# Kernel optimization log

Hardware: AMD Instinct MI355X
Metric: run time of the kernel (lower is better)

The kernel has to match this reference:

```python
import jax, jax.numpy as jnp
import numpy as np

N = 50000          # nodes
E = 800000         # edges (before self-loops)
DIN = 1024         # input_dim_mel
HID = 128          # hidden_dim
HEADS = 2
NC = 4             # num_classes
NEG_SLOPE = 0.2    # PyG GATConv default


def setup_inputs() -> dict:
    key = jax.random.key(0)
    ks = jax.random.split(key, 12)
    s = 0.05
    return {
        "x": jax.random.normal(ks[0], (N, DIN), dtype=jnp.float32),
        "edge_index": jax.random.randint(ks[1], (2, E), 0, N, dtype=jnp.int64),
        # linear_pre (stored as [in, out])
        "W_pre": jax.random.normal(ks[2], (DIN, HID), dtype=jnp.float32) * s,
        "b_pre": jnp.zeros((HID,), dtype=jnp.float32),
        # gat1: GATConv(HID, HID, heads=2, concat=True)
        "W1": jax.random.normal(ks[3], (HID, HEADS * HID), dtype=jnp.float32) * s,
        "a_src1": jax.random.normal(ks[4], (HEADS, HID), dtype=jnp.float32) * s,
        "a_dst1": jax.random.normal(ks[5], (HEADS, HID), dtype=jnp.float32) * s,
        "b1": jnp.zeros((HEADS * HID,), dtype=jnp.float32),
        # gat2: GATConv(HID*HEADS, NC, heads=1, concat=True)
        "W2": jax.random.normal(ks[6], (HEADS * HID, NC), dtype=jnp.float32) * s,
        "a_src2": jax.random.normal(ks[7], (1, NC), dtype=jnp.float32) * s,
        "a_dst2": jax.random.normal(ks[8], (1, NC), dtype=jnp.float32) * s,
        "b2": jnp.zeros((NC,), dtype=jnp.float32),
    }


def _gat_conv(x, W, a_src, a_dst, bias, src, dst, heads, out_ch):
    """PyG GATConv (concat=True, self-loops already appended to src/dst)."""
    n = x.shape[0]
    h = (x @ W).reshape(n, heads, out_ch)            # [N,H,C]
    alpha_src = (h * a_src).sum(-1)                  # [N,H]
    alpha_dst = (h * a_dst).sum(-1)                  # [N,H]
    e = alpha_src[src] + alpha_dst[dst]              # [E,H] edge scores
    e = jax.nn.leaky_relu(e, NEG_SLOPE)
    # segment softmax over incoming edges of each dst node
    m = jax.ops.segment_max(e, dst, num_segments=n)  # [N,H]
    e = jnp.exp(e - m[dst])
    s = jax.ops.segment_sum(e, dst, num_segments=n)  # [N,H]
    alpha = e / (s[dst] + 1e-16)                     # [E,H]
    # gather src messages, weight by attention, scatter-add to dst
    out = jax.ops.segment_sum(h[src] * alpha[:, :, None], dst, num_segments=n)
    return out.reshape(n, heads * out_ch) + bias


def reference(x, edge_index, W_pre, b_pre, W1, a_src1, a_dst1, b1,
              W2, a_src2, a_dst2, b2):
    n = x.shape[0]
    # add self-loops (PyG GATConv default)
    loops = jnp.arange(n, dtype=edge_index.dtype)
    src = jnp.concatenate([edge_index[0], loops])
    dst = jnp.concatenate([edge_index[1], loops])

    h = jax.nn.relu(x @ W_pre + b_pre)                               # [N,HID]
    h = jax.nn.elu(_gat_conv(h, W1, a_src1, a_dst1, b1, src, dst, HEADS, HID))
    out = _gat_conv(h, W2, a_src2, a_dst2, b2, src, dst, 1, NC)      # [N,NC]
    return out
```

## Files before the change

kernel.cpp:

```cpp
#include <hip/hip_runtime.h>
#include <hip/hip_bf16.h>

#define NEG_SLOPE 0.2f

typedef _Float16 f16x8 __attribute__((ext_vector_type(8)));
typedef _Float16 f16x4 __attribute__((ext_vector_type(4)));
typedef float f32x4 __attribute__((ext_vector_type(4)));
typedef unsigned short ushort_t;

#define AS_GLOBAL(p) ((const __attribute__((address_space(1))) void*)(p))
#define AS_SHARED(p) ((__attribute__((address_space(3))) void*)(p))


__global__ void khist(const int* __restrict__ dst, int E, int* __restrict__ counts) {
    int i = blockIdx.x * blockDim.x + threadIdx.x;
    if (i < E) atomicAdd(&counts[dst[i]], 1);
}

__global__ __launch_bounds__(1024) void kscan_part(const int* __restrict__ counts,
                                                   int* __restrict__ row_ptr,
                                                   int* __restrict__ bsum, int n) {
    __shared__ int wsum[16];
    int t = threadIdx.x, lane = t & 63, wid = t >> 6;
    int i = blockIdx.x * 1024 + t;
    int v = (i < n) ? (counts[i] + 1) : 0;
    int x = v;
    #pragma unroll
    for (int off = 1; off < 64; off <<= 1) {
        int y = __shfl_up(x, off, 64);
        if (lane >= off) x += y;
    }
    if (lane == 63) wsum[wid] = x;
    __syncthreads();
    if (wid == 0) {
        int ws = (lane < 16) ? wsum[lane] : 0;
        #pragma unroll
        for (int off = 1; off < 16; off <<= 1) {
            int y = __shfl_up(ws, off, 64);
            if (lane >= off) ws += y;
        }
        if (lane < 16) wsum[lane] = ws;
    }
    __syncthreads();
    int wave_excl = (wid == 0) ? 0 : wsum[wid - 1];
    if (i < n) row_ptr[i] = wave_excl + (x - v);
    if (t == 0) bsum[blockIdx.x] = wsum[15];
}

__global__ void kscan_tops(const int* __restrict__ bsum, int* __restrict__ boff,
                           int* __restrict__ row_ptr, int G, int n) {
    int lane = threadIdx.x;
    int v = (lane < G) ? bsum[lane] : 0;
    int x = v;
    #pragma unroll
    for (int off = 1; off < 64; off <<= 1) {
        int y = __shfl_up(x, off, 64);
        if (lane >= off) x += y;
    }
    if (lane < G) boff[lane] = x - v;
    if (lane == 63) row_ptr[n] = x;
}

__global__ void kscan_add(int* __restrict__ row_ptr, const int* __restrict__ boff,
                          int* __restrict__ cursor, int n) {
    int i = blockIdx.x * blockDim.x + threadIdx.x;
    if (i < n) {
        int r = row_ptr[i] + boff[i >> 10];
        row_ptr[i] = r;
        cursor[i] = r;
    }
}

__global__ void kfill(const int* __restrict__ src, const int* __restrict__ dst,
                      int E, int n, int* __restrict__ cursor, int* __restrict__ edge_src) {
    int i = blockIdx.x * blockDim.x + threadIdx.x;
    if (i < E) {
        int p = atomicAdd(&cursor[dst[i]], 1);
        edge_src[p] = src[i];
    } else if (i < E + n) {
        int v = i - E;
        int p = atomicAdd(&cursor[v], 1);
        edge_src[p] = v;
    }
}

__global__ void kprep(const float* __restrict__ Wpre, const float* __restrict__ W1,
                      ushort_t* __restrict__ PreF, ushort_t* __restrict__ W1h) {
    int i = blockIdx.x * blockDim.x + threadIdx.x;
    if (i < 1024 * 128) {
        int k = i >> 7, n = i & 127;
        int d = ((k >> 3) * 128 + n) * 8 + (k & 7);
        PreF[d] = __builtin_bit_cast(ushort_t, (_Float16)Wpre[i]);
    } else if (i < 1024 * 128 + 128 * 256) {
        int j2 = i - 1024 * 128;
        int k = j2 >> 8, n = j2 & 255;
        int d = ((k >> 3) * 256 + n) * 8 + (k & 7);
        W1h[d] = __builtin_bit_cast(ushort_t, (_Float16)W1[j2]);
    }
}

__device__ inline f16x4 cvt4(float4 v) {
    f16x4 r;
    r[0] = (_Float16)v.x; r[1] = (_Float16)v.y;
    r[2] = (_Float16)v.z; r[3] = (_Float16)v.w;
    return r;
}

__global__ __launch_bounds__(256) void kgemm_mfma1(const float* __restrict__ A,
                                                   const ushort_t* __restrict__ Bf,
                                                   const float* __restrict__ bias,
                                                   ushort_t* __restrict__ C, int M) {
    __shared__ __align__(16) ushort_t Bs[8192];
    __shared__ __align__(16) ushort_t As[2048];
    int t = threadIdx.x;
    int wid = t >> 6, lane = t & 63, q = lane >> 4, l15 = lane & 15;
    int wr = wid & 1, wc = wid >> 1;
    int m0 = blockIdx.x * 32;

    int ar = t >> 3, ac = t & 7;
    int srow = m0 + ar;
    if (srow >= M) srow = M - 1;
    const float* sA = A + (size_t)srow * 1024;
    int sw = ar & 7;
    int wadr0 = ar * 64 + (((ac >> 1)) ^ sw) * 8 + (ac & 1) * 4;
    int wadr1 = ar * 64 + ((4 + (ac >> 1)) ^ sw) * 8 + (ac & 1) * 4;

    float4 av[2][2];
    av[0][0] = *(const float4*)(sA + ac * 4);
    av[0][1] = *(const float4*)(sA + 32 + ac * 4);

    f32x4 acc[4];
    #pragma unroll
    for (int c = 0; c < 4; ++c) acc[c] = (f32x4){0.f, 0.f, 0.f, 0.f};

    int arow_rd = (wr * 16 + l15) * 64;
    int asw = l15 & 7;

    #pragma unroll 2
    for (int kt = 0; kt < 16; ++kt) {
        int cur = kt & 1, nxt = cur ^ 1;
        __syncthreads();
        {
            const ushort_t* sF = Bf + kt * 8192;
            #pragma unroll
            for (int i = 0; i < 4; ++i) {
                int ge = (i * 256 + t) * 8;
                int le = (i * 256 + (t & 0xC0)) * 8;
                __builtin_amdgcn_global_load_lds(AS_GLOBAL(sF + ge), AS_SHARED(Bs + le), 16, 0, 0);
            }
        }
        if (kt < 15) {
            const float* a2 = sA + (kt + 1) * 64;
            av[nxt][0] = *(const float4*)(a2 + ac * 4);
            av[nxt][1] = *(const float4*)(a2 + 32 + ac * 4);
        }
        *(f16x4*)(As + wadr0) = cvt4(av[cur][0]);
        *(f16x4*)(As + wadr1) = cvt4(av[cur][1]);
        __syncthreads();
        #pragma unroll
        for (int ks = 0; ks < 2; ++ks) {
            int kc = ks * 4 + q;
            f16x8 af = *(const f16x8*)(As + arow_rd + ((kc ^ asw) * 8));
            #pragma unroll
            for (int c = 0; c < 4; ++c) {
                f16x8 b = *(const f16x8*)(Bs + (kc * 128 + wc * 64 + c * 16 + l15) * 8);
                acc[c] = __builtin_amdgcn_mfma_f32_16x16x32_f16(af, b, acc[c], 0, 0, 0);
            }
        }
    }
    #pragma unroll
    for (int c = 0; c < 4; ++c) {
        int n = wc * 64 + c * 16 + l15;
        float bv = bias[n];
        #pragma unroll
        for (int r = 0; r < 4; ++r) {
            int mm = m0 + wr * 16 + q * 4 + r;
            if (mm < M)
                C[(size_t)mm * 128 + n] =
                    __builtin_bit_cast(ushort_t, (_Float16)fmaxf(acc[c][r] + bv, 0.f));
        }
    }
}

__global__ __launch_bounds__(256) void kgemm_mfma2(const ushort_t* __restrict__ Ah,
                                                   const ushort_t* __restrict__ W1h,
                                                   const float* __restrict__ a_src,
                                                   const float* __restrict__ a_dst,
                                                   ushort_t* __restrict__ C,
                                                   float* __restrict__ as1,
                                                   float* __restrict__ ad1, int M) {
    __shared__ __align__(16) ushort_t Bs[16384];
    int t = threadIdx.x;
    int wid = t >> 6, lane = t & 63;
    int q = lane >> 4, l15 = lane & 15;
    int g = blockIdx.y;
    int m0 = blockIdx.x * 64 + wid * 16;
    int m = m0 + l15;
    const ushort_t* arow = Ah + (size_t)(m < M ? m : 0) * 128;

    {
        #pragma unroll
        for (int i = 0; i < 8; ++i) {
            int j = i * 4 + wid;
            int kc = j >> 1, hk = j & 1;
            int ge = ((kc * 256) + g * 128 + hk * 64 + lane) * 8;
            int le = j * 512;
            __builtin_amdgcn_global_load_lds(AS_GLOBAL(W1h + ge), AS_SHARED(Bs + le), 16, 0, 0);
        }
    }
    f16x8 af[4];
    #pragma unroll
    for (int ks = 0; ks < 4; ++ks)
        af[ks] = *(const f16x8*)(arow + ks * 32 + q * 8);
    __syncthreads();

    f32x4 acc[8];
    #pragma unroll
    for (int c = 0; c < 8; ++c) acc[c] = (f32x4){0.f, 0.f, 0.f, 0.f};

    #pragma unroll
    for (int ks = 0; ks < 4; ++ks) {
        int kc = ks * 4 + q;
        #pragma unroll
        for (int c = 0; c < 8; ++c) {
            f16x8 b = *(const f16x8*)(Bs + (kc * 128 + c * 16 + l15) * 8);
            acc[c] = __builtin_amdgcn_mfma_f32_16x16x32_f16(af[ks], b, acc[c], 0, 0, 0);
        }
    }
    #pragma unroll
    for (int c = 0; c < 8; ++c) {
        int n = g * 128 + c * 16 + l15;
        #pragma unroll
        for (int r = 0; r < 4; ++r) {
            int mm = m0 + q * 4 + r;
            if (mm < M)
                C[(size_t)mm * 256 + n] = __builtin_bit_cast(ushort_t, (_Float16)acc[c][r]);
        }
    }
    float asv[4] = {0.f, 0.f, 0.f, 0.f};
    float adv[4] = {0.f, 0.f, 0.f, 0.f};
    #pragma unroll
    for (int c = 0; c < 8; ++c) {
        float sa = a_src[g * 128 + c * 16 + l15];
        float da = a_dst[g * 128 + c * 16 + l15];
        #pragma unroll
        for (int r = 0; r < 4; ++r) {
            asv[r] += acc[c][r] * sa;
            adv[r] += acc[c][r] * da;
        }
    }
    #pragma unroll
    for (int off = 1; off <= 8; off <<= 1) {
        #pragma unroll
        for (int r = 0; r < 4; ++r) {
            asv[r] += __shfl_xor(asv[r], off, 64);
            adv[r] += __shfl_xor(adv[r], off, 64);
        }
    }
    if (l15 == 0) {
        #pragma unroll
        for (int r = 0; r < 4; ++r) {
            int node = m0 + q * 4 + r;
            if (node < M) {
                as1[node * 2 + g] = asv[r];
                ad1[node * 2 + g] = adv[r];
            }
        }
    }
}

__global__ __launch_bounds__(128) void kagg1(const ushort_t* __restrict__ h1h,
                                             const float* __restrict__ as1,
                                             const float* __restrict__ ad1,
                                             const float* __restrict__ b1,
                                             const float* __restrict__ W2,
                                             const float* __restrict__ a_src2,
                                             const float* __restrict__ a_dst2,
                                             const int* __restrict__ row_ptr,
                                             const int* __restrict__ edge_src,
                                             float* __restrict__ h2,
                                             float* __restrict__ as2,
                                             float* __restrict__ ad2, int n) {
    __shared__ float w_lds[128];
    __shared__ int   s_lds[64];
    __shared__ float red[2][4];
    int node = blockIdx.x;
    int t = threadIdx.x;
    int wid = t >> 6;
    int beg = row_ptr[node], end = row_ptr[node + 1];
    int h_ch = t >> 6;
    float advv = ad1[node * 2 + (t & 1)];
    float acc0 = 0.f, acc1 = 0.f, ssum = 0.f;
    for (int base = beg; base < end; base += 64) {
        int cnt = min(64, end - base);
        int i = t >> 1, h = t & 1;
        if (i < cnt) {
            int s = edge_src[base + i];
            float e = as1[s * 2 + h] + advv;
            e = (e > 0.f) ? e : NEG_SLOPE * e;
            w_lds[i * 2 + h] = __expf(e);
            if (h == 0) s_lds[i] = s;
        }
        __syncthreads();
        #pragma unroll 4
        for (int i2 = 0; i2 < cnt; ++i2) {
            float wv = w_lds[i2 * 2 + h_ch];
            int s = s_lds[i2];
            unsigned p = *(const unsigned*)(h1h + (size_t)s * 256 + t * 2);
            _Float16 lo16 = __builtin_bit_cast(_Float16, (ushort_t)(p & 0xffffu));
            _Float16 hi16 = __builtin_bit_cast(_Float16, (ushort_t)(p >> 16));
            acc0 += wv * (float)lo16;
            acc1 += wv * (float)hi16;
            ssum += wv;
        }
        __syncthreads();
    }
    float inv = 1.f / (ssum + 1e-16f);
    float o0 = acc0 * inv + b1[t * 2];
    float o1 = acc1 * inv + b1[t * 2 + 1];
    o0 = (o0 > 0.f) ? o0 : (__expf(o0) - 1.f);
    o1 = (o1 > 0.f) ? o1 : (__expf(o1) - 1.f);
    float4 w0 = *(const float4*)(W2 + t * 8);
    float4 w1 = *(const float4*)(W2 + t * 8 + 4);
    float p0 = o0 * w0.x + o1 * w1.x;
    float p1 = o0 * w0.y + o1 * w1.y;
    float p2 = o0 * w0.z + o1 * w1.z;
    float p3 = o0 * w0.w + o1 * w1.w;
    #pragma unroll
    for (int off = 1; off < 64; off <<= 1) {
        p0 += __shfl_xor(p0, off, 64);
        p1 += __shfl_xor(p1, off, 64);
        p2 += __shfl_xor(p2, off, 64);
        p3 += __shfl_xor(p3, off, 64);
    }
    if ((t & 63) == 0) {
        red[wid][0] = p0; red[wid][1] = p1; red[wid][2] = p2; red[wid][3] = p3;
    }
    __syncthreads();
    if (t == 0) {
        float hv[4], s2 = 0.f, d2 = 0.f;
        #pragma unroll
        for (int j = 0; j < 4; ++j) {
            hv[j] = red[0][j] + red[1][j];
            h2[node * 4 + j] = hv[j];
            s2 += hv[j] * a_src2[j];
            d2 += hv[j] * a_dst2[j];
        }
        as2[node] = s2;
        ad2[node] = d2;
    }
}

__global__ __launch_bounds__(256) void kagg2(const float* __restrict__ h2,
                                             const float* __restrict__ as2,
                                             const float* __restrict__ ad2,
                                             const float* __restrict__ b2,
                                             const int* __restrict__ row_ptr,
                                             const int* __restrict__ edge_src,
                                             float* __restrict__ out, int n) {
    int wid = threadIdx.x >> 6, lane = threadIdx.x & 63;
    int node = blockIdx.x * 4 + wid;
    if (node >= n) return;
    int beg = row_ptr[node], end = row_ptr[node + 1];
    int j = lane & 3, ig = lane >> 2;
    float adv = ad2[node];
    float acc = 0.f, ssum = 0.f;
    for (int p = beg + ig; p < end; p += 16) {
        int s = edge_src[p];
        float e = as2[s] + adv;
        e = (e > 0.f) ? e : NEG_SLOPE * e;
        float wv = __expf(e);
        acc += wv * h2[s * 4 + j];
        ssum += wv;
    }
    #pragma unroll
    for (int off = 32; off >= 4; off >>= 1) {
        acc += __shfl_down(acc, off);
        ssum += __shfl_down(ssum, off);
    }
    if (lane < 4) out[node * 4 + j] = acc / (ssum + 1e-16f) + b2[j];
}

extern "C" void kernel_launch(void* const* d_in, const int* in_sizes, int n_in,
                              void* d_out, int out_size, void* d_ws, size_t ws_size,
                              hipStream_t stream) {
    const float* x      = (const float*)d_in[0];
    const int*   ei     = (const int*)d_in[1];
    const float* W_pre  = (const float*)d_in[2];
    const float* b_pre  = (const float*)d_in[3];
    const float* W1     = (const float*)d_in[4];
    const float* a_src1 = (const float*)d_in[5];
    const float* a_dst1 = (const float*)d_in[6];
    const float* b1     = (const float*)d_in[7];
    const float* W2     = (const float*)d_in[8];
    const float* a_src2 = (const float*)d_in[9];
    const float* a_dst2 = (const float*)d_in[10];
    const float* b2     = (const float*)d_in[11];
    float* out = (float*)d_out;

    const int DIN = 1024;
    const int E = in_sizes[1] / 2;
    const int N = in_sizes[0] / DIN;

    const int* esrc = ei;
    const int* edst = ei + E;

    char* ws = (char*)d_ws;
    size_t off = 0;
    ushort_t* h1h = (ushort_t*)(ws + off); off += (size_t)N * 256 * 2;
    ushort_t* h0h = (ushort_t*)(ws + off); off += (size_t)N * 128 * 2;
    float* as1 = (float*)(ws + off);  off += (size_t)N * 2 * 4;
    float* ad1 = (float*)(ws + off);  off += (size_t)N * 2 * 4;
    float* h2  = (float*)(ws + off);  off += (size_t)N * 4 * 4;
    float* as2 = (float*)(ws + off);  off += (size_t)N * 4;
    float* ad2 = (float*)(ws + off);  off += (size_t)N * 4;
    int* row_ptr = (int*)(ws + off);  off += ((size_t)N + 16) * 4;
    int* cursor  = (int*)(ws + off);  off += (size_t)N * 4;
    int* counts  = (int*)(ws + off);  off += (size_t)N * 4;
    int* bsum    = (int*)(ws + off);  off += 64 * 4;
    int* boff    = (int*)(ws + off);  off += 64 * 4;
    int* edge_src = (int*)(ws + off); off += (size_t)(E + N) * 4;
    ushort_t* PreF = (ushort_t*)(ws + off); off += 1024 * 128 * 2;
    ushort_t* W1h  = (ushort_t*)(ws + off); off += 128 * 256 * 2;

    int G = (N + 1023) / 1024;

    kprep<<<640, 256, 0, stream>>>(W_pre, W1, PreF, W1h);
    hipMemsetAsync(counts, 0, (size_t)N * 4, stream);
    khist<<<(E + 255) / 256, 256, 0, stream>>>(edst, E, counts);
    kscan_part<<<G, 1024, 0, stream>>>(counts, row_ptr, bsum, N);
    kscan_tops<<<1, 64, 0, stream>>>(bsum, boff, row_ptr, G, N);
    kscan_add<<<(N + 255) / 256, 256, 0, stream>>>(row_ptr, boff, cursor, N);
    kfill<<<(E + N + 255) / 256, 256, 0, stream>>>(esrc, edst, E, N, cursor, edge_src);

    int Mb32 = (N + 31) / 32;
    kgemm_mfma1<<<Mb32, 256, 0, stream>>>(x, PreF, b_pre, h0h, N);
    {
        int Mb = (N + 63) / 64;
        dim3 grid(Mb, 2);
        kgemm_mfma2<<<grid, 256, 0, stream>>>(h0h, W1h, a_src1, a_dst1, h1h, as1, ad1, N);
    }
    kagg1<<<N, 128, 0, stream>>>(h1h, as1, ad1, b1, W2, a_src2, a_dst2,
                                 row_ptr, edge_src, h2, as2, ad2, N);
    kagg2<<<(N + 3) / 4, 256, 0, stream>>>(h2, as2, ad2, b2, row_ptr, edge_src, out, N);
}
```

Before: 521.6 us.

## Process one node per wavefront in GAT layer-1 aggregation using shuffles

The first aggregation kernel now assigns one 64-lane wavefront per destination node instead of a 128-thread block. Each lane gathers four fp16 channels with an 8-byte load, and edge weights and source indices are broadcast with wave shuffles instead of LDS. This removes block-level barriers and the LDS reduction, and packs four nodes per 256-thread block to cut block scheduling overhead. Each lane now holds more accumulators, and the gather per edge stays a single 512-byte row read.

```diff
diff --git a/kernel.cpp b/kernel.cpp
--- a/kernel.cpp
+++ b/kernel.cpp
@@ -269,7 +269,7 @@
     }
 }
 
-__global__ __launch_bounds__(128) void kagg1(const ushort_t* __restrict__ h1h,
+__global__ __launch_bounds__(256) void kagg1(const ushort_t* __restrict__ h1h,
                                              const float* __restrict__ as1,
                                              const float* __restrict__ ad1,
                                              const float* __restrict__ b1,
@@ -281,51 +281,56 @@
                                              float* __restrict__ h2,
                                              float* __restrict__ as2,
                                              float* __restrict__ ad2, int n) {
-    __shared__ float w_lds[128];
-    __shared__ int   s_lds[64];
-    __shared__ float red[2][4];
-    int node = blockIdx.x;
-    int t = threadIdx.x;
-    int wid = t >> 6;
+    int wid = threadIdx.x >> 6, lane = threadIdx.x & 63;
+    int node = blockIdx.x * 4 + wid;
+    if (node >= n) return;
     int beg = row_ptr[node], end = row_ptr[node + 1];
-    int h_ch = t >> 6;
-    float advv = ad1[node * 2 + (t & 1)];
-    float acc0 = 0.f, acc1 = 0.f, ssum = 0.f;
-    for (int base = beg; base < end; base += 64) {
-        int cnt = min(64, end - base);
-        int i = t >> 1, h = t & 1;
-        if (i < cnt) {
-            int s = edge_src[base + i];
-            float e = as1[s * 2 + h] + advv;
-            e = (e > 0.f) ? e : NEG_SLOPE * e;
-            w_lds[i * 2 + h] = __expf(e);
-            if (h == 0) s_lds[i] = s;
-        }
-        __syncthreads();
+    int h = lane >> 5;
+    float adv0 = ad1[node * 2];
+    float adv1 = ad1[node * 2 + 1];
+    float acc0 = 0.f, acc1 = 0.f, acc2 = 0.f, acc3 = 0.f, ssum = 0.f;
+    for (int base = beg; base < end; base += 32) {
+        int cnt = min(32, end - base);
+        float wv_mine = 0.f;
+        int s_mine = 0;
+        {
+            int i = lane >> 1, hh = lane & 1;
+            if (i < cnt) {
+                s_mine = edge_src[base + i];
+                float e = as1[s_mine * 2 + hh] + (hh ? adv1 : adv0);
+                e = (e > 0.f) ? e : NEG_SLOPE * e;
+                wv_mine = __expf(e);
+            }
+        }
         #pragma unroll 4
         for (int i2 = 0; i2 < cnt; ++i2) {
-            float wv = w_lds[i2 * 2 + h_ch];
-            int s = s_lds[i2];
-            unsigned p = *(const unsigned*)(h1h + (size_t)s * 256 + t * 2);
-            _Float16 lo16 = __builtin_bit_cast(_Float16, (ushort_t)(p & 0xffffu));
-            _Float16 hi16 = __builtin_bit_cast(_Float16, (ushort_t)(p >> 16));
-            acc0 += wv * (float)lo16;
-            acc1 += wv * (float)hi16;
+            int s = __shfl(s_mine, i2 * 2, 64);
+            float wv = __shfl(wv_mine, i2 * 2 + h, 64);
+            uint2 p = *(const uint2*)(h1h + (size_t)s * 256 + lane * 4);
+            acc0 += wv * (float)__builtin_bit_cast(_Float16, (ushort_t)(p.x & 0xffffu));
+            acc1 += wv * (float)__builtin_bit_cast(_Float16, (ushort_t)(p.x >> 16));
+            acc2 += wv * (float)__builtin_bit_cast(_Float16, (ushort_t)(p.y & 0xffffu));
+            acc3 += wv * (float)__builtin_bit_cast(_Float16, (ushort_t)(p.y >> 16));
             ssum += wv;
         }
-        __syncthreads();
     }
     float inv = 1.f / (ssum + 1e-16f);
-    float o0 = acc0 * inv + b1[t * 2];
-    float o1 = acc1 * inv + b1[t * 2 + 1];
+    float o0 = acc0 * inv + b1[lane * 4 + 0];
+    float o1 = acc1 * inv + b1[lane * 4 + 1];
+    float o2 = acc2 * inv + b1[lane * 4 + 2];
+    float o3 = acc3 * inv + b1[lane * 4 + 3];
     o0 = (o0 > 0.f) ? o0 : (__expf(o0) - 1.f);
     o1 = (o1 > 0.f) ? o1 : (__expf(o1) - 1.f);
-    float4 w0 = *(const float4*)(W2 + t * 8);
-    float4 w1 = *(const float4*)(W2 + t * 8 + 4);
-    float p0 = o0 * w0.x + o1 * w1.x;
-    float p1 = o0 * w0.y + o1 * w1.y;
-    float p2 = o0 * w0.z + o1 * w1.z;
-    float p3 = o0 * w0.w + o1 * w1.w;
+    o2 = (o2 > 0.f) ? o2 : (__expf(o2) - 1.f);
+    o3 = (o3 > 0.f) ? o3 : (__expf(o3) - 1.f);
+    float4 w0 = *(const float4*)(W2 + (lane * 4 + 0) * 4);
+    float4 w1 = *(const float4*)(W2 + (lane * 4 + 1) * 4);
+    float4 w2 = *(const float4*)(W2 + (lane * 4 + 2) * 4);
+    float4 w3 = *(const float4*)(W2 + (lane * 4 + 3) * 4);
+    float p0 = o0 * w0.x + o1 * w1.x + o2 * w2.x + o3 * w3.x;
+    float p1 = o0 * w0.y + o1 * w1.y + o2 * w2.y + o3 * w3.y;
+    float p2 = o0 * w0.z + o1 * w1.z + o2 * w2.z + o3 * w3.z;
+    float p3 = o0 * w0.w + o1 * w1.w + o2 * w2.w + o3 * w3.w;
     #pragma unroll
     for (int off = 1; off < 64; off <<= 1) {
         p0 += __shfl_xor(p0, off, 64);
@@ -333,21 +338,13 @@
         p2 += __shfl_xor(p2, off, 64);
         p3 += __shfl_xor(p3, off, 64);
     }
-    if ((t & 63) == 0) {
-        red[wid][0] = p0; red[wid][1] = p1; red[wid][2] = p2; red[wid][3] = p3;
-    }
-    __syncthreads();
-    if (t == 0) {
-        float hv[4], s2 = 0.f, d2 = 0.f;
-        #pragma unroll
-        for (int j = 0; j < 4; ++j) {
-            hv[j] = red[0][j] + red[1][j];
-            h2[node * 4 + j] = hv[j];
-            s2 += hv[j] * a_src2[j];
-            d2 += hv[j] * a_dst2[j];
-        }
-        as2[node] = s2;
-        ad2[node] = d2;
+    if (lane == 0) {
+        h2[node * 4 + 0] = p0;
+        h2[node * 4 + 1] = p1;
+        h2[node * 4 + 2] = p2;
+        h2[node * 4 + 3] = p3;
+        as2[node] = p0 * a_src2[0] + p1 * a_src2[1] + p2 * a_src2[2] + p3 * a_src2[3];
+        ad2[node] = p0 * a_dst2[0] + p1 * a_dst2[1] + p2 * a_dst2[2] + p3 * a_dst2[3];
     }
 }
 
@@ -440,7 +437,7 @@
         dim3 grid(Mb, 2);
         kgemm_mfma2<<<grid, 256, 0, stream>>>(h0h, W1h, a_src1, a_dst1, h1h, as1, ad1, N);
     }
-    kagg1<<<N, 128, 0, stream>>>(h1h, as1, ad1, b1, W2, a_src2, a_dst2,
-                                 row_ptr, edge_src, h2, as2, ad2, N);
+    kagg1<<<(N + 3) / 4, 256, 0, stream>>>(h1h, as1, ad1, b1, W2, a_src2, a_dst2,
+                                           row_ptr, edge_src, h2, as2, ad2, N);
     kagg2<<<(N + 3) / 4, 256, 0, stream>>>(h2, as2, ad2, b2, row_ptr, edge_src, out, N);
 }
```

After: 536.1 us. 1.03x slower.
